# Performance work log

Hardware: AMD Instinct MI355X
Metric: run time of the kernel (lower is better)

The kernel has to match this reference:

```python
import jax, jax.numpy as jnp
import numpy as np

EPS = 1e-10
B, N, F, H, C = 4, 512, 64, 64, 32


def _lin_init(key, fan_in, fan_out):
    return jax.random.normal(key, (fan_in, fan_out), dtype=jnp.float32) / np.sqrt(fan_in)


def setup_inputs() -> dict:
    key = jax.random.key(0)
    ks = jax.random.split(key, 12)
    inp = {
        "h": jax.random.normal(ks[0], (B, N, F), dtype=jnp.float32),
        "x": jax.random.normal(ks[1], (B, N, 3), dtype=jnp.float32),
        "mask": jnp.ones((B, N, N), dtype=jnp.float32),
        # edge_model (ConcatenationFilter): Linear(2F+1,H) SiLU Linear(H,H) SiLU
        "We1": _lin_init(ks[2], 2 * F + 1, H), "be1": jnp.zeros((H,), jnp.float32),
        "We2": _lin_init(ks[3], H, H), "be2": jnp.zeros((H,), jnp.float32),
        # coefficients_mlp: Linear(H,H) SiLU Linear(H,C)
        "Wc1": _lin_init(ks[4], H, H), "bc1": jnp.zeros((H,), jnp.float32),
        "Wc2": _lin_init(ks[5], H, C), "bc2": jnp.zeros((C,), jnp.float32),
        # post_norm_mlp: Linear(C,H) SiLU Linear(H,H)
        "Wp1": _lin_init(ks[6], C, H), "bp1": jnp.zeros((H,), jnp.float32),
        "Wp2": _lin_init(ks[7], H, H), "bp2": jnp.zeros((H,), jnp.float32),
        # node_mlp: Linear(2H+F,H) SiLU Linear(H,F)
        "Wn1": _lin_init(ks[8], 2 * H + F, H), "bn1": jnp.zeros((H,), jnp.float32),
        "Wn2": _lin_init(ks[9], H, F), "bn2": jnp.zeros((F,), jnp.float32),
    }
    return inp


def _forward(h, x, mask, We1, be1, We2, be2, Wc1, bc1, Wc2, bc2,
             Wp1, bp1, Wp2, bp2, Wn1, bn1, Wn2, bn2):
    b, n, f = h.shape
    # pairwise displacements: entry (i, j) = x_j - x_i  -> [B,N,N,3]
    x_minus_xt = x[..., None, :, :] - x[..., :, None, :]
    # squared pairwise distance (norm with eps=0, then squared) -> [B,N,N,1]
    norm2 = jnp.sum(x_minus_xt * x_minus_xt, axis=-1, keepdims=True)
    # h_cat_ht: [h_i broadcast over j dim order per get_h_cat_h] -> [B,N,N,2F]
    hi = jnp.broadcast_to(h[..., None, :, :], (b, n, n, f))
    hj = jnp.broadcast_to(h[..., :, None, :], (b, n, n, f))
    edge_in = jnp.concatenate([hi, hj, norm2], axis=-1)  # [B,N,N,2F+1]
    # ConcatenationFilter edge model
    h_e_mtx = jax.nn.silu(jax.nn.silu(edge_in @ We1 + be1) @ We2 + be2)  # [B,N,N,H]
    # aggregate (masked sum over neighbor dim -2)
    h_e = jnp.sum(h_e_mtx * mask[..., None], axis=-2)  # [B,N,H]
    # spatial attention
    coeff = jax.nn.silu(h_e_mtx @ Wc1 + bc1) @ Wc2 + bc2  # [B,N,N,C]
    vec = x_minus_xt / (norm2 ** 2.0 + EPS)  # [B,N,N,3]
    # combinations = coeff[...,c,None] * vec[...,None,:]; masked sum over dim -3 (j)
    comb_sum = jnp.einsum("bijc,bijd,bij->bicd", coeff, vec, mask)  # [B,N,C,3]
    comb_norm = jnp.sum(comb_sum * comb_sum, axis=-1)  # [B,N,C]
    h_comb = jax.nn.silu(comb_norm @ Wp1 + bp1) @ Wp2 + bp2  # [B,N,H]
    # node model with residual
    node_in = jnp.concatenate([h, h_e, h_comb], axis=-1)  # [B,N,F+2H]
    out = jax.nn.silu(node_in @ Wn1 + bn1) @ Wn2 + bn2  # [B,N,F]
    h_new = h + out
    return h_new


def reference(h, x, mask, We1, be1, We2, be2, Wc1, bc1, Wc2, bc2,
              Wp1, bp1, Wp2, bp2, Wn1, bn1, Wn2, bn2):
    h_new = _forward(h, x, mask, We1, be1, We2, be2, Wc1, bc1, Wc2, bc2,
                     Wp1, bp1, Wp2, bp2, Wn1, bn1, Wn2, bn2)
    # update_coordinate=False: x passes through unchanged
    return (h_new, x)
```

## Files before the change

kernel.cpp:

```cpp
#include <hip/hip_runtime.h>

#define BB 4
#define NN 512
#define FF 64

typedef __attribute__((ext_vector_type(8))) _Float16 half8v;
typedef __attribute__((ext_vector_type(4))) float f32x4;

__device__ __forceinline__ float silu_f(float v) {
  return v * __builtin_amdgcn_rcpf(1.0f + __expf(-v));
}
__device__ __forceinline__ unsigned cvt_pk_f16(float a, float b) {
  auto r = __builtin_amdgcn_cvt_pkrtz(a, b);
  unsigned u; __builtin_memcpy(&u, &r, 4); return u;
}
__device__ __forceinline__ unsigned short f2h(float w) {
  _Float16 hf = (_Float16)w;
  unsigned short us; __builtin_memcpy(&us, &hf, 2); return us;
}

#define AIDX(j, k) ((((j) << 6)) | (((((k) >> 3) ^ ((j) & 7))) << 3) | ((k) & 7))

__global__ void sake_prep(const float* __restrict__ h, const float* __restrict__ We1,
                          const float* __restrict__ be1, const float* __restrict__ We2,
                          const float* __restrict__ Wc1, const float* __restrict__ Wc2,
                          float* __restrict__ G, float* __restrict__ Base,
                          unsigned short* __restrict__ w2f,
                          unsigned short* __restrict__ w3f,
                          unsigned short* __restrict__ w4f)
{
  const int wg = (int)blockIdx.x, tid = (int)threadIdx.x;
  if (wg < 64) {
    __shared__ float sH[32][64];
    const int r0 = wg * 32;
    for (int idx = tid; idx < 2048; idx += 256) sH[idx >> 6][idx & 63] = h[r0 * 64 + idx];
    __syncthreads();
    const int rl = tid >> 3;
    const int o0 = (tid & 7) * 8;
    float aG[8], aB[8];
    #pragma unroll
    for (int o = 0; o < 8; ++o) { aG[o] = 0.f; aB[o] = be1[o0 + o]; }
    for (int k = 0; k < 64; ++k) {
      const float hv = sH[rl][k];
      const float4 g0 = *(const float4*)&We1[k * 64 + o0];
      const float4 g1 = *(const float4*)&We1[k * 64 + o0 + 4];
      const float4 b0 = *(const float4*)&We1[(64 + k) * 64 + o0];
      const float4 b1 = *(const float4*)&We1[(64 + k) * 64 + o0 + 4];
      aG[0] = fmaf(hv, g0.x, aG[0]); aG[1] = fmaf(hv, g0.y, aG[1]);
      aG[2] = fmaf(hv, g0.z, aG[2]); aG[3] = fmaf(hv, g0.w, aG[3]);
      aG[4] = fmaf(hv, g1.x, aG[4]); aG[5] = fmaf(hv, g1.y, aG[5]);
      aG[6] = fmaf(hv, g1.z, aG[6]); aG[7] = fmaf(hv, g1.w, aG[7]);
      aB[0] = fmaf(hv, b0.x, aB[0]); aB[1] = fmaf(hv, b0.y, aB[1]);
      aB[2] = fmaf(hv, b0.z, aB[2]); aB[3] = fmaf(hv, b0.w, aB[3]);
      aB[4] = fmaf(hv, b1.x, aB[4]); aB[5] = fmaf(hv, b1.y, aB[5]);
      aB[6] = fmaf(hv, b1.z, aB[6]); aB[7] = fmaf(hv, b1.w, aB[7]);
    }
    const size_t base = (size_t)(r0 + rl) * 64 + o0;
    *(float4*)&G[base]        = make_float4(aG[0], aG[1], aG[2], aG[3]);
    *(float4*)&G[base + 4]    = make_float4(aG[4], aG[5], aG[6], aG[7]);
    *(float4*)&Base[base]     = make_float4(aB[0], aB[1], aB[2], aB[3]);
    *(float4*)&Base[base + 4] = make_float4(aB[4], aB[5], aB[6], aB[7]);
  } else {
    for (int idx = tid; idx < 10240; idx += 256) {
      float w; unsigned short* pf; int pos;
      if (idx < 4096)      { const int o = idx >> 6,          k = idx & 63;
                             w = We2[k * 64 + o]; pf = w2f; pos = o * 64 + k; }
      else if (idx < 8192) { const int t = idx - 4096, o = t >> 6, k = t & 63;
                             w = Wc1[k * 64 + o]; pf = w3f; pos = o * 64 + k; }
      else                 { const int t = idx - 8192, c = t >> 6, k = t & 63;
                             w = Wc2[k * 32 + c]; pf = w4f; pos = c * 64 + k; }
      pf[pos] = f2h(w);
    }
  }
}

__device__ __forceinline__ void pack_store4(unsigned short* sA, int a,
                                            float v0, float v1, float v2, float v3) {
  *(uint2*)&sA[a] = make_uint2(cvt_pk_f16(v0, v1), cvt_pk_f16(v2, v3));
}

__global__ __launch_bounds__(256, 3)
void sake_mfma(const float* __restrict__ h, const float* __restrict__ x,
               const float* __restrict__ mask,
               const float* __restrict__ We1, const float* __restrict__ be2,
               const float* __restrict__ bc1, const float* __restrict__ bc2,
               const float* __restrict__ Wp1, const float* __restrict__ bp1,
               const float* __restrict__ Wp2, const float* __restrict__ bp2,
               const float* __restrict__ Wn1, const float* __restrict__ bn1,
               const float* __restrict__ Wn2, const float* __restrict__ bn2,
               const float* __restrict__ G, const float* __restrict__ Base,
               const unsigned short* __restrict__ w2f,
               const unsigned short* __restrict__ w3f,
               const unsigned short* __restrict__ w4f,
               float* __restrict__ out)
{
  __shared__ unsigned short sAct[2 * 8192];
  __shared__ float sMaskL[128];
  __shared__ float sBase[64], sW1n[64], sHi[64];
  __shared__ float sB2[64], sB3[64], sB4[32];
  __shared__ float sHe[64], sCombP[4][48], sCN[32], sTmp[64], sHcomb[64];

  const int tid  = (int)threadIdx.x;
  const int blk  = (int)blockIdx.x;
  const int b    = blk >> 9;
  const int i    = blk & 511;
  const int lane = tid & 63;
  const int wid  = tid >> 6;
  const int l15  = lane & 15;
  const int lg   = lane >> 4;
  const int mb   = wid * 16;
  const int m2   = wid & 1;
  const int jh   = (wid >> 1) * 16;

  const size_t mrow = ((size_t)(b * NN + i)) * NN;

  if (tid < 64) {
    sBase[tid] = Base[((size_t)(b * NN + i)) * 64 + tid];
    sW1n[tid]  = We1[128 * 64 + tid];
    sHi[tid]   = h[((size_t)(b * NN + i)) * 64 + tid];
    sB2[tid]   = be2[tid];
    sB3[tid]   = bc1[tid];
  }
  if (tid < 32) sB4[tid] = bc2[tid];
  const float xi0 = x[((size_t)(b * NN + i)) * 3 + 0];
  const float xi1 = x[((size_t)(b * NN + i)) * 3 + 1];
  const float xi2 = x[((size_t)(b * NN + i)) * 3 + 2];

  half8v w2F[2], w3F[2], w4F[2];
  #pragma unroll
  for (int ks = 0; ks < 2; ++ks) {
    const int ko = ks * 32 + lg * 8;
    w2F[ks] = *(const half8v*)&w2f[(mb + l15) * 64 + ko];
    w3F[ks] = *(const half8v*)&w3f[(mb + l15) * 64 + ko];
    w4F[ks] = *(const half8v*)&w4f[(m2 * 16 + l15) * 64 + ko];
  }

  float heAcc[4] = {0.f, 0.f, 0.f, 0.f};
  float cAcc[4][3] = {};

  __syncthreads();

  for (int jt = 0; jt < 4; ++jt) {
    const int jb = jt * 128;

    #pragma unroll
    for (int jj = 0; jj < 2; ++jj) {
      const int jloc = jj * 64 + wid * 16 + l15;
      const int j = jb + jloc;
      const size_t xo = ((size_t)(b * NN + j)) * 3;
      const float dx = x[xo + 0] - xi0;
      const float dy = x[xo + 1] - xi1;
      const float dz = x[xo + 2] - xi2;
      const float n2 = dx * dx + dy * dy + dz * dz;
      if (lg == 0) sMaskL[jloc] = mask[mrow + j];
      #pragma unroll
      for (int kk = 0; kk < 4; ++kk) {
        const int kb = lg * 16 + kk * 4;
        const float4 g4 = *(const float4*)&G[((size_t)(b * NN + j)) * 64 + kb];
        const float4 bs = *(const float4*)&sBase[kb];
        const float4 wn = *(const float4*)&sW1n[kb];
        const float v0 = silu_f(g4.x + bs.x + n2 * wn.x);
        const float v1 = silu_f(g4.y + bs.y + n2 * wn.y);
        const float v2 = silu_f(g4.z + bs.z + n2 * wn.z);
        const float v3 = silu_f(g4.w + bs.w + n2 * wn.w);
        pack_store4(sAct, AIDX(jloc, kb), v0, v1, v2, v3);
      }
    }
    __syncthreads();

    {
      const f32x4 bias = *(const f32x4*)&sB2[mb + lg * 4];
      #pragma unroll
      for (int nf = 0; nf < 8; ++nf) {
        const int jn = nf * 16 + l15;
        f32x4 acc = bias;
        #pragma unroll
        for (int ks = 0; ks < 2; ++ks) {
          const half8v bh = *(const half8v*)&sAct[AIDX(jn, ks * 32 + lg * 8)];
          acc = __builtin_amdgcn_mfma_f32_16x16x32_f16(w2F[ks], bh, acc, 0, 0, 0);
        }
        const float m = sMaskL[jn];
        float v[4];
        #pragma unroll
        for (int r = 0; r < 4; ++r) { v[r] = silu_f(acc[r]); heAcc[r] = fmaf(v[r], m, heAcc[r]); }
        pack_store4(sAct, 8192 + AIDX(jn, mb + lg * 4), v[0], v[1], v[2], v[3]);
      }
    }
    __syncthreads();

    {
      const f32x4 bias = *(const f32x4*)&sB3[mb + lg * 4];
      #pragma unroll
      for (int nf = 0; nf < 8; ++nf) {
        const int jn = nf * 16 + l15;
        f32x4 acc = bias;
        #pragma unroll
        for (int ks = 0; ks < 2; ++ks) {
          const half8v bh = *(const half8v*)&sAct[8192 + AIDX(jn, ks * 32 + lg * 8)];
          acc = __builtin_amdgcn_mfma_f32_16x16x32_f16(w3F[ks], bh, acc, 0, 0, 0);
        }
        float v[4];
        #pragma unroll
        for (int r = 0; r < 4; ++r) v[r] = silu_f(acc[r]);
        pack_store4(sAct, AIDX(jn, mb + lg * 4), v[0], v[1], v[2], v[3]);
      }
    }
    __syncthreads();

    {
      const f32x4 bias = *(const f32x4*)&sB4[m2 * 16 + lg * 4];
      #pragma unroll
      for (int jj = 0; jj < 4; ++jj) {
        const int jloc = jj * 32 + jh + l15;
        const int j = jb + jloc;
        const size_t xo = ((size_t)(b * NN + j)) * 3;
        const float dx = x[xo + 0] - xi0;
        const float dy = x[xo + 1] - xi1;
        const float dz = x[xo + 2] - xi2;
        const float n2 = dx * dx + dy * dy + dz * dz;
        const float inv = __builtin_amdgcn_rcpf(n2 * n2 + 1e-10f);
        const float m = mask[mrow + j];
        const float vm0 = dx * inv * m, vm1 = dy * inv * m, vm2 = dz * inv * m;
        const half8v bh0 = *(const half8v*)&sAct[AIDX(jloc, lg * 8)];
        const half8v bh1 = *(const half8v*)&sAct[AIDX(jloc, 32 + lg * 8)];
        f32x4 acc = bias;
        acc = __builtin_amdgcn_mfma_f32_16x16x32_f16(w4F[0], bh0, acc, 0, 0, 0);
        acc = __builtin_amdgcn_mfma_f32_16x16x32_f16(w4F[1], bh1, acc, 0, 0, 0);
        #pragma unroll
        for (int r = 0; r < 4; ++r) {
          cAcc[r][0] = fmaf(acc[r], vm0, cAcc[r][0]);
          cAcc[r][1] = fmaf(acc[r], vm1, cAcc[r][1]);
          cAcc[r][2] = fmaf(acc[r], vm2, cAcc[r][2]);
        }
      }
    }
    __syncthreads();
  }

  #pragma unroll
  for (int r = 0; r < 4; ++r) {
    float s = heAcc[r];
    s += __shfl_xor(s, 1); s += __shfl_xor(s, 2); s += __shfl_xor(s, 4); s += __shfl_xor(s, 8);
    if (l15 == 0) sHe[mb + lg * 4 + r] = s;
  }
  #pragma unroll
  for (int r = 0; r < 4; ++r)
    #pragma unroll
    for (int d = 0; d < 3; ++d) {
      float s = cAcc[r][d];
      s += __shfl_xor(s, 1); s += __shfl_xor(s, 2); s += __shfl_xor(s, 4); s += __shfl_xor(s, 8);
      if (l15 == 0) sCombP[wid][(lg * 4 + r) * 3 + d] = s;
    }
  __syncthreads();
  if (tid < 32) {
    const int c = tid, cm2 = c >> 4, cl = c & 15;
    const float s0 = sCombP[cm2][cl * 3 + 0] + sCombP[cm2 + 2][cl * 3 + 0];
    const float s1 = sCombP[cm2][cl * 3 + 1] + sCombP[cm2 + 2][cl * 3 + 1];
    const float s2 = sCombP[cm2][cl * 3 + 2] + sCombP[cm2 + 2][cl * 3 + 2];
    sCN[c] = s0 * s0 + s1 * s1 + s2 * s2;
  }
  __syncthreads();

  if (tid < 64) {
    float s = bp1[tid];
    #pragma unroll 8
    for (int c = 0; c < 32; ++c) s = fmaf(sCN[c], Wp1[c * 64 + tid], s);
    sTmp[tid] = silu_f(s);
  }
  __syncthreads();
  if (tid < 64) {
    float s = bp2[tid];
    #pragma unroll 16
    for (int k = 0; k < 64; ++k) s = fmaf(sTmp[k], Wp2[k * 64 + tid], s);
    sHcomb[tid] = s;
  }
  __syncthreads();
  if (tid < 64) {
    float s = bn1[tid];
    #pragma unroll 16
    for (int m = 0; m < 64; ++m) s = fmaf(sHi[m],    Wn1[m * 64 + tid],         s);
    #pragma unroll 16
    for (int m = 0; m < 64; ++m) s = fmaf(sHe[m],    Wn1[(64 + m) * 64 + tid],  s);
    #pragma unroll 16
    for (int m = 0; m < 64; ++m) s = fmaf(sHcomb[m], Wn1[(128 + m) * 64 + tid], s);
    sTmp[tid] = silu_f(s);
  }
  __syncthreads();
  if (tid < 64) {
    float s = bn2[tid];
    #pragma unroll 16
    for (int k = 0; k < 64; ++k) s = fmaf(sTmp[k], Wn2[k * 64 + tid], s);
    out[((size_t)(b * NN + i)) * 64 + tid] = sHi[tid] + s;
  } else if (tid < 67) {
    const int d = tid - 64;
    out[(size_t)BB * NN * FF + ((size_t)(b * NN + i)) * 3 + d] = x[((size_t)(b * NN + i)) * 3 + d];
  }
}

extern "C" void kernel_launch(void* const* d_in, const int* in_sizes, int n_in,
                              void* d_out, int out_size, void* d_ws, size_t ws_size,
                              hipStream_t stream) {
  const float* h    = (const float*)d_in[0];
  const float* x    = (const float*)d_in[1];
  const float* mask = (const float*)d_in[2];
  const float* We1  = (const float*)d_in[3];
  const float* be1  = (const float*)d_in[4];
  const float* We2  = (const float*)d_in[5];
  const float* be2  = (const float*)d_in[6];
  const float* Wc1  = (const float*)d_in[7];
  const float* bc1  = (const float*)d_in[8];
  const float* Wc2  = (const float*)d_in[9];
  const float* bc2  = (const float*)d_in[10];
  const float* Wp1  = (const float*)d_in[11];
  const float* bp1  = (const float*)d_in[12];
  const float* Wp2  = (const float*)d_in[13];
  const float* bp2  = (const float*)d_in[14];
  const float* Wn1  = (const float*)d_in[15];
  const float* bn1  = (const float*)d_in[16];
  const float* Wn2  = (const float*)d_in[17];
  const float* bn2  = (const float*)d_in[18];
  float* out = (float*)d_out;

  float* G    = (float*)d_ws;
  float* Base = G + 2048 * 64;
  unsigned short* w2f = (unsigned short*)(Base + 2048 * 64);
  unsigned short* w3f = w2f + 4096;
  unsigned short* w4f = w3f + 4096;

  hipLaunchKernelGGL(sake_prep, dim3(65), dim3(256), 0, stream,
                     h, We1, be1, We2, Wc1, Wc2, G, Base, w2f, w3f, w4f);
  hipLaunchKernelGGL(sake_mfma, dim3(BB * NN), dim3(256), 0, stream,
                     h, x, mask, We1, be2, bc1, bc2,
                     Wp1, bp1, Wp2, bp2, Wn1, bn1, Wn2, bn2,
                     G, Base, w2f, w3f, w4f, out);
}
```

Before: 107.6 us.

## Assign one row per wave and remove block-wide barriers from the edge loop

Restructures the main kernel so each wave processes a full output row i, with four rows per workgroup, looping over neighbours in 16-wide tiles. Intermediate activations stay in per-wave LDS scratch, so the j loop needs no __syncthreads, and the fp16 weight matrices are staged once per block in shared memory. The aim is to remove barrier stalls and improve overlap between MFMA and elementwise work. The cost is more LDS traffic for weight fragments and higher register use from larger per-wave accumulators.

```diff
diff --git a/kernel.cpp b/kernel.cpp
--- a/kernel.cpp
+++ b/kernel.cpp
@@ -17,6 +17,10 @@
 __device__ __forceinline__ unsigned short f2h(float w) {
   _Float16 hf = (_Float16)w;
   unsigned short us; __builtin_memcpy(&us, &hf, 2); return us;
+}
+__device__ __forceinline__ half8v mk_half8(unsigned u0, unsigned u1, unsigned u2, unsigned u3) {
+  uint4 uu = make_uint4(u0, u1, u2, u3);
+  half8v r; __builtin_memcpy(&r, &uu, 16); return r;
 }
 
 #define AIDX(j, k) ((((j) << 6)) | (((((k) >> 3) ^ ((j) & 7))) << 3) | ((k) & 7))
@@ -74,13 +78,8 @@
   }
 }
 
-__device__ __forceinline__ void pack_store4(unsigned short* sA, int a,
-                                            float v0, float v1, float v2, float v3) {
-  *(uint2*)&sA[a] = make_uint2(cvt_pk_f16(v0, v1), cvt_pk_f16(v2, v3));
-}
-
 __global__ __launch_bounds__(256, 3)
-void sake_mfma(const float* __restrict__ h, const float* __restrict__ x,
+void sake_wave(const float* __restrict__ h, const float* __restrict__ x,
                const float* __restrict__ mask,
                const float* __restrict__ We1, const float* __restrict__ be2,
                const float* __restrict__ bc1, const float* __restrict__ bc2,
@@ -94,206 +93,181 @@
                const unsigned short* __restrict__ w4f,
                float* __restrict__ out)
 {
-  __shared__ unsigned short sAct[2 * 8192];
-  __shared__ float sMaskL[128];
-  __shared__ float sBase[64], sW1n[64], sHi[64];
-  __shared__ float sB2[64], sB3[64], sB4[32];
-  __shared__ float sHe[64], sCombP[4][48], sCN[32], sTmp[64], sHcomb[64];
+  __shared__ unsigned short sW2[4096], sW3[4096], sW4[2048];
+  __shared__ float sB2[64], sB3[64], sB4[32], sW1n[64];
+  __shared__ float sBaseW[4][64], sHiW[4][64];
+  __shared__ unsigned short sActA[4][1024], sActB[4][1024];
+  __shared__ float sHeW[4][64], sCombW[4][96], sCNW[4][32];
+  __shared__ float sTmpW[4][64], sHcombW[4][64];
 
   const int tid  = (int)threadIdx.x;
   const int blk  = (int)blockIdx.x;
-  const int b    = blk >> 9;
-  const int i    = blk & 511;
+  const int wid  = tid >> 6;
   const int lane = tid & 63;
-  const int wid  = tid >> 6;
   const int l15  = lane & 15;
   const int lg   = lane >> 4;
-  const int mb   = wid * 16;
-  const int m2   = wid & 1;
-  const int jh   = (wid >> 1) * 16;
-
-  const size_t mrow = ((size_t)(b * NN + i)) * NN;
-
-  if (tid < 64) {
-    sBase[tid] = Base[((size_t)(b * NN + i)) * 64 + tid];
-    sW1n[tid]  = We1[128 * 64 + tid];
-    sHi[tid]   = h[((size_t)(b * NN + i)) * 64 + tid];
-    sB2[tid]   = be2[tid];
-    sB3[tid]   = bc1[tid];
-  }
-  if (tid < 32) sB4[tid] = bc2[tid];
-  const float xi0 = x[((size_t)(b * NN + i)) * 3 + 0];
-  const float xi1 = x[((size_t)(b * NN + i)) * 3 + 1];
-  const float xi2 = x[((size_t)(b * NN + i)) * 3 + 2];
-
-  half8v w2F[2], w3F[2], w4F[2];
+  const int row  = blk * 4 + wid;
+  const int b    = row >> 9;
+  const int i    = row & 511;
+
+  const size_t mrow = ((size_t)row) * NN;
+
+  for (int idx = tid; idx < 2048; idx += 256) ((uint*)sW2)[idx] = ((const uint*)w2f)[idx];
+  for (int idx = tid; idx < 2048; idx += 256) ((uint*)sW3)[idx] = ((const uint*)w3f)[idx];
+  for (int idx = tid; idx < 1024; idx += 256) ((uint*)sW4)[idx] = ((const uint*)w4f)[idx];
+  if (tid < 64) { sB2[tid] = be2[tid]; sB3[tid] = bc1[tid]; sW1n[tid] = We1[128 * 64 + tid]; }
+  if (tid >= 64 && tid < 96) sB4[tid - 64] = bc2[tid - 64];
+  sBaseW[wid][lane] = Base[((size_t)row) * 64 + lane];
+  sHiW[wid][lane]   = h[((size_t)row) * 64 + lane];
+  const float xi0 = x[((size_t)row) * 3 + 0];
+  const float xi1 = x[((size_t)row) * 3 + 1];
+  const float xi2 = x[((size_t)row) * 3 + 2];
+  __syncthreads();
+
+  float heAcc[4][4] = {};
+  float cAcc[2][4][3] = {};
+
+  for (int jt = 0; jt < 32; ++jt) {
+    const int j = jt * 16 + l15;
+    const size_t xo = ((size_t)(b * NN + j)) * 3;
+    const float dx = x[xo + 0] - xi0;
+    const float dy = x[xo + 1] - xi1;
+    const float dz = x[xo + 2] - xi2;
+    const float n2 = dx * dx + dy * dy + dz * dz;
+    const float inv = __builtin_amdgcn_rcpf(n2 * n2 + 1e-10f);
+    const float m = mask[mrow + j];
+    const float vm0 = dx * inv * m, vm1 = dy * inv * m, vm2 = dz * inv * m;
+
+    half8v a1[2];
+    #pragma unroll
+    for (int ks = 0; ks < 2; ++ks) {
+      const int kb = ks * 32 + lg * 8;
+      const float4 g0 = *(const float4*)&G[((size_t)(b * NN + j)) * 64 + kb];
+      const float4 g1 = *(const float4*)&G[((size_t)(b * NN + j)) * 64 + kb + 4];
+      const f32x4 bs0 = *(const f32x4*)&sBaseW[wid][kb];
+      const f32x4 bs1 = *(const f32x4*)&sBaseW[wid][kb + 4];
+      const f32x4 wn0 = *(const f32x4*)&sW1n[kb];
+      const f32x4 wn1 = *(const f32x4*)&sW1n[kb + 4];
+      const float v0 = silu_f(g0.x + bs0[0] + n2 * wn0[0]);
+      const float v1 = silu_f(g0.y + bs0[1] + n2 * wn0[1]);
+      const float v2 = silu_f(g0.z + bs0[2] + n2 * wn0[2]);
+      const float v3 = silu_f(g0.w + bs0[3] + n2 * wn0[3]);
+      const float v4 = silu_f(g1.x + bs1[0] + n2 * wn1[0]);
+      const float v5 = silu_f(g1.y + bs1[1] + n2 * wn1[1]);
+      const float v6 = silu_f(g1.z + bs1[2] + n2 * wn1[2]);
+      const float v7 = silu_f(g1.w + bs1[3] + n2 * wn1[3]);
+      a1[ks] = mk_half8(cvt_pk_f16(v0, v1), cvt_pk_f16(v2, v3),
+                        cvt_pk_f16(v4, v5), cvt_pk_f16(v6, v7));
+    }
+
+    #pragma unroll
+    for (int fb = 0; fb < 4; ++fb) {
+      f32x4 acc = *(const f32x4*)&sB2[fb * 16 + lg * 4];
+      #pragma unroll
+      for (int ks = 0; ks < 2; ++ks) {
+        const half8v wA = *(const half8v*)&sW2[(fb * 16 + l15) * 64 + ks * 32 + lg * 8];
+        acc = __builtin_amdgcn_mfma_f32_16x16x32_f16(wA, a1[ks], acc, 0, 0, 0);
+      }
+      float v[4];
+      #pragma unroll
+      for (int r = 0; r < 4; ++r) { v[r] = silu_f(acc[r]); heAcc[fb][r] = fmaf(v[r], m, heAcc[fb][r]); }
+      *(uint2*)&sActA[wid][AIDX(l15, fb * 16 + lg * 4)] =
+          make_uint2(cvt_pk_f16(v[0], v[1]), cvt_pk_f16(v[2], v[3]));
+    }
+    half8v a2[2];
+    a2[0] = *(const half8v*)&sActA[wid][AIDX(l15, lg * 8)];
+    a2[1] = *(const half8v*)&sActA[wid][AIDX(l15, 32 + lg * 8)];
+
+    #pragma unroll
+    for (int fb = 0; fb < 4; ++fb) {
+      f32x4 acc = *(const f32x4*)&sB3[fb * 16 + lg * 4];
+      #pragma unroll
+      for (int ks = 0; ks < 2; ++ks) {
+        const half8v wA = *(const half8v*)&sW3[(fb * 16 + l15) * 64 + ks * 32 + lg * 8];
+        acc = __builtin_amdgcn_mfma_f32_16x16x32_f16(wA, a2[ks], acc, 0, 0, 0);
+      }
+      float v[4];
+      #pragma unroll
+      for (int r = 0; r < 4; ++r) v[r] = silu_f(acc[r]);
+      *(uint2*)&sActB[wid][AIDX(l15, fb * 16 + lg * 4)] =
+          make_uint2(cvt_pk_f16(v[0], v[1]), cvt_pk_f16(v[2], v[3]));
+    }
+    half8v a3[2];
+    a3[0] = *(const half8v*)&sActB[wid][AIDX(l15, lg * 8)];
+    a3[1] = *(const half8v*)&sActB[wid][AIDX(l15, 32 + lg * 8)];
+
+    #pragma unroll
+    for (int cb = 0; cb < 2; ++cb) {
+      f32x4 acc = *(const f32x4*)&sB4[cb * 16 + lg * 4];
+      #pragma unroll
+      for (int ks = 0; ks < 2; ++ks) {
+        const half8v wA = *(const half8v*)&sW4[(cb * 16 + l15) * 64 + ks * 32 + lg * 8];
+        acc = __builtin_amdgcn_mfma_f32_16x16x32_f16(wA, a3[ks], acc, 0, 0, 0);
+      }
+      #pragma unroll
+      for (int r = 0; r < 4; ++r) {
+        cAcc[cb][r][0] = fmaf(acc[r], vm0, cAcc[cb][r][0]);
+        cAcc[cb][r][1] = fmaf(acc[r], vm1, cAcc[cb][r][1]);
+        cAcc[cb][r][2] = fmaf(acc[r], vm2, cAcc[cb][r][2]);
+      }
+    }
+  }
+
   #pragma unroll
-  for (int ks = 0; ks < 2; ++ks) {
-    const int ko = ks * 32 + lg * 8;
-    w2F[ks] = *(const half8v*)&w2f[(mb + l15) * 64 + ko];
-    w3F[ks] = *(const half8v*)&w3f[(mb + l15) * 64 + ko];
-    w4F[ks] = *(const half8v*)&w4f[(m2 * 16 + l15) * 64 + ko];
-  }
-
-  float heAcc[4] = {0.f, 0.f, 0.f, 0.f};
-  float cAcc[4][3] = {};
-
-  __syncthreads();
-
-  for (int jt = 0; jt < 4; ++jt) {
-    const int jb = jt * 128;
-
-    #pragma unroll
-    for (int jj = 0; jj < 2; ++jj) {
-      const int jloc = jj * 64 + wid * 16 + l15;
-      const int j = jb + jloc;
-      const size_t xo = ((size_t)(b * NN + j)) * 3;
-      const float dx = x[xo + 0] - xi0;
-      const float dy = x[xo + 1] - xi1;
-      const float dz = x[xo + 2] - xi2;
-      const float n2 = dx * dx + dy * dy + dz * dz;
-      if (lg == 0) sMaskL[jloc] = mask[mrow + j];
-      #pragma unroll
-      for (int kk = 0; kk < 4; ++kk) {
-        const int kb = lg * 16 + kk * 4;
-        const float4 g4 = *(const float4*)&G[((size_t)(b * NN + j)) * 64 + kb];
-        const float4 bs = *(const float4*)&sBase[kb];
-        const float4 wn = *(const float4*)&sW1n[kb];
-        const float v0 = silu_f(g4.x + bs.x + n2 * wn.x);
-        const float v1 = silu_f(g4.y + bs.y + n2 * wn.y);
-        const float v2 = silu_f(g4.z + bs.z + n2 * wn.z);
-        const float v3 = silu_f(g4.w + bs.w + n2 * wn.w);
-        pack_store4(sAct, AIDX(jloc, kb), v0, v1, v2, v3);
-      }
-    }
-    __syncthreads();
-
-    {
-      const f32x4 bias = *(const f32x4*)&sB2[mb + lg * 4];
-      #pragma unroll
-      for (int nf = 0; nf < 8; ++nf) {
-        const int jn = nf * 16 + l15;
-        f32x4 acc = bias;
-        #pragma unroll
-        for (int ks = 0; ks < 2; ++ks) {
-          const half8v bh = *(const half8v*)&sAct[AIDX(jn, ks * 32 + lg * 8)];
-          acc = __builtin_amdgcn_mfma_f32_16x16x32_f16(w2F[ks], bh, acc, 0, 0, 0);
-        }
-        const float m = sMaskL[jn];
-        float v[4];
-        #pragma unroll
-        for (int r = 0; r < 4; ++r) { v[r] = silu_f(acc[r]); heAcc[r] = fmaf(v[r], m, heAcc[r]); }
-        pack_store4(sAct, 8192 + AIDX(jn, mb + lg * 4), v[0], v[1], v[2], v[3]);
-      }
-    }
-    __syncthreads();
-
-    {
-      const f32x4 bias = *(const f32x4*)&sB3[mb + lg * 4];
-      #pragma unroll
-      for (int nf = 0; nf < 8; ++nf) {
-        const int jn = nf * 16 + l15;
-        f32x4 acc = bias;
-        #pragma unroll
-        for (int ks = 0; ks < 2; ++ks) {
-          const half8v bh = *(const half8v*)&sAct[8192 + AIDX(jn, ks * 32 + lg * 8)];
-          acc = __builtin_amdgcn_mfma_f32_16x16x32_f16(w3F[ks], bh, acc, 0, 0, 0);
-        }
-        float v[4];
-        #pragma unroll
-        for (int r = 0; r < 4; ++r) v[r] = silu_f(acc[r]);
-        pack_store4(sAct, AIDX(jn, mb + lg * 4), v[0], v[1], v[2], v[3]);
-      }
-    }
-    __syncthreads();
-
-    {
-      const f32x4 bias = *(const f32x4*)&sB4[m2 * 16 + lg * 4];
-      #pragma unroll
-      for (int jj = 0; jj < 4; ++jj) {
-        const int jloc = jj * 32 + jh + l15;
-        const int j = jb + jloc;
-        const size_t xo = ((size_t)(b * NN + j)) * 3;
-        const float dx = x[xo + 0] - xi0;
-        const float dy = x[xo + 1] - xi1;
-        const float dz = x[xo + 2] - xi2;
-        const float n2 = dx * dx + dy * dy + dz * dz;
-        const float inv = __builtin_amdgcn_rcpf(n2 * n2 + 1e-10f);
-        const float m = mask[mrow + j];
-        const float vm0 = dx * inv * m, vm1 = dy * inv * m, vm2 = dz * inv * m;
-        const half8v bh0 = *(const half8v*)&sAct[AIDX(jloc, lg * 8)];
-        const half8v bh1 = *(const half8v*)&sAct[AIDX(jloc, 32 + lg * 8)];
-        f32x4 acc = bias;
-        acc = __builtin_amdgcn_mfma_f32_16x16x32_f16(w4F[0], bh0, acc, 0, 0, 0);
-        acc = __builtin_amdgcn_mfma_f32_16x16x32_f16(w4F[1], bh1, acc, 0, 0, 0);
-        #pragma unroll
-        for (int r = 0; r < 4; ++r) {
-          cAcc[r][0] = fmaf(acc[r], vm0, cAcc[r][0]);
-          cAcc[r][1] = fmaf(acc[r], vm1, cAcc[r][1]);
-          cAcc[r][2] = fmaf(acc[r], vm2, cAcc[r][2]);
-        }
-      }
-    }
-    __syncthreads();
-  }
-
+  for (int fb = 0; fb < 4; ++fb)
+    #pragma unroll
+    for (int r = 0; r < 4; ++r) {
+      float s = heAcc[fb][r];
+      s += __shfl_xor(s, 1); s += __shfl_xor(s, 2); s += __shfl_xor(s, 4); s += __shfl_xor(s, 8);
+      if (l15 == 0) sHeW[wid][fb * 16 + lg * 4 + r] = s;
+    }
   #pragma unroll
-  for (int r = 0; r < 4; ++r) {
-    float s = heAcc[r];
-    s += __shfl_xor(s, 1); s += __shfl_xor(s, 2); s += __shfl_xor(s, 4); s += __shfl_xor(s, 8);
-    if (l15 == 0) sHe[mb + lg * 4 + r] = s;
-  }
-  #pragma unroll
-  for (int r = 0; r < 4; ++r)
-    #pragma unroll
-    for (int d = 0; d < 3; ++d) {
-      float s = cAcc[r][d];
-      s += __shfl_xor(s, 1); s += __shfl_xor(s, 2); s += __shfl_xor(s, 4); s += __shfl_xor(s, 8);
-      if (l15 == 0) sCombP[wid][(lg * 4 + r) * 3 + d] = s;
-    }
-  __syncthreads();
-  if (tid < 32) {
-    const int c = tid, cm2 = c >> 4, cl = c & 15;
-    const float s0 = sCombP[cm2][cl * 3 + 0] + sCombP[cm2 + 2][cl * 3 + 0];
-    const float s1 = sCombP[cm2][cl * 3 + 1] + sCombP[cm2 + 2][cl * 3 + 1];
-    const float s2 = sCombP[cm2][cl * 3 + 2] + sCombP[cm2 + 2][cl * 3 + 2];
-    sCN[c] = s0 * s0 + s1 * s1 + s2 * s2;
-  }
-  __syncthreads();
-
-  if (tid < 64) {
-    float s = bp1[tid];
+  for (int cb = 0; cb < 2; ++cb)
+    #pragma unroll
+    for (int r = 0; r < 4; ++r)
+      #pragma unroll
+      for (int d = 0; d < 3; ++d) {
+        float s = cAcc[cb][r][d];
+        s += __shfl_xor(s, 1); s += __shfl_xor(s, 2); s += __shfl_xor(s, 4); s += __shfl_xor(s, 8);
+        if (l15 == 0) sCombW[wid][(cb * 16 + lg * 4 + r) * 3 + d] = s;
+      }
+  if (lane < 32) {
+    const int c = lane;
+    const float s0 = sCombW[wid][c * 3 + 0];
+    const float s1 = sCombW[wid][c * 3 + 1];
+    const float s2 = sCombW[wid][c * 3 + 2];
+    sCNW[wid][c] = s0 * s0 + s1 * s1 + s2 * s2;
+  }
+  {
+    float s = bp1[lane];
     #pragma unroll 8
-    for (int c = 0; c < 32; ++c) s = fmaf(sCN[c], Wp1[c * 64 + tid], s);
-    sTmp[tid] = silu_f(s);
-  }
-  __syncthreads();
-  if (tid < 64) {
-    float s = bp2[tid];
-    #pragma unroll 16
-    for (int k = 0; k < 64; ++k) s = fmaf(sTmp[k], Wp2[k * 64 + tid], s);
-    sHcomb[tid] = s;
-  }
-  __syncthreads();
-  if (tid < 64) {
-    float s = bn1[tid];
-    #pragma unroll 16
-    for (int m = 0; m < 64; ++m) s = fmaf(sHi[m],    Wn1[m * 64 + tid],         s);
-    #pragma unroll 16
-    for (int m = 0; m < 64; ++m) s = fmaf(sHe[m],    Wn1[(64 + m) * 64 + tid],  s);
-    #pragma unroll 16
-    for (int m = 0; m < 64; ++m) s = fmaf(sHcomb[m], Wn1[(128 + m) * 64 + tid], s);
-    sTmp[tid] = silu_f(s);
-  }
-  __syncthreads();
-  if (tid < 64) {
-    float s = bn2[tid];
-    #pragma unroll 16
-    for (int k = 0; k < 64; ++k) s = fmaf(sTmp[k], Wn2[k * 64 + tid], s);
-    out[((size_t)(b * NN + i)) * 64 + tid] = sHi[tid] + s;
-  } else if (tid < 67) {
-    const int d = tid - 64;
-    out[(size_t)BB * NN * FF + ((size_t)(b * NN + i)) * 3 + d] = x[((size_t)(b * NN + i)) * 3 + d];
+    for (int c = 0; c < 32; ++c) s = fmaf(sCNW[wid][c], Wp1[c * 64 + lane], s);
+    sTmpW[wid][lane] = silu_f(s);
+  }
+  {
+    float s = bp2[lane];
+    #pragma unroll 16
+    for (int k = 0; k < 64; ++k) s = fmaf(sTmpW[wid][k], Wp2[k * 64 + lane], s);
+    sHcombW[wid][lane] = s;
+  }
+  {
+    float s = bn1[lane];
+    #pragma unroll 16
+    for (int mm = 0; mm < 64; ++mm) s = fmaf(sHiW[wid][mm],    Wn1[mm * 64 + lane],         s);
+    #pragma unroll 16
+    for (int mm = 0; mm < 64; ++mm) s = fmaf(sHeW[wid][mm],    Wn1[(64 + mm) * 64 + lane],  s);
+    #pragma unroll 16
+    for (int mm = 0; mm < 64; ++mm) s = fmaf(sHcombW[wid][mm], Wn1[(128 + mm) * 64 + lane], s);
+    sTmpW[wid][lane] = silu_f(s);
+  }
+  {
+    float s = bn2[lane];
+    #pragma unroll 16
+    for (int k = 0; k < 64; ++k) s = fmaf(sTmpW[wid][k], Wn2[k * 64 + lane], s);
+    out[((size_t)row) * 64 + lane] = sHiW[wid][lane] + s;
+  }
+  if (lane < 3) {
+    out[(size_t)BB * NN * FF + ((size_t)row) * 3 + lane] = x[((size_t)row) * 3 + lane];
   }
 }
 
@@ -329,7 +303,7 @@
 
   hipLaunchKernelGGL(sake_prep, dim3(65), dim3(256), 0, stream,
                      h, We1, be1, We2, Wc1, Wc2, G, Base, w2f, w3f, w4f);
-  hipLaunchKernelGGL(sake_mfma, dim3(BB * NN), dim3(256), 0, stream,
+  hipLaunchKernelGGL(sake_wave, dim3(BB * NN / 4), dim3(256), 0, stream,
                      h, x, mask, We1, be2, bc1, bc2,
                      Wp1, bp1, Wp2, bp2, Wn1, bn1, Wn2, bn2,
                      G, Base, w2f, w3f, w4f, out);
```

Result: slower. 249.3 us (+131.8%).
